# Kernel tuning notes

Measured on AMD Instinct MI355X. Metric: run time of the kernel, lower is better.

Reference implementation:

```python
import jax, jax.numpy as jnp
import numpy as np

NUM_COARSE = 1024

def sqdist(a, b):
    # a: [..., N, 3], b: [..., M, 3] -> [..., N, M] squared euclidean distances
    d = (jnp.sum(a * a, -1)[..., :, None] + jnp.sum(b * b, -1)[..., None, :]
         - 2.0 * jnp.einsum('...nd,...md->...nm', a, b))
    return jnp.maximum(d, 0.0)

def fps_idx(pts, n_samples):
    # pts: [N, 3]; farthest point sampling starting from index 0 (pn2 convention)
    d0 = jnp.sum((pts - pts[0]) ** 2, -1)  # [N]
    def step(dists, _):
        idx = jnp.argmax(dists)
        d = jnp.sum((pts - pts[idx]) ** 2, -1)
        return jnp.minimum(dists, d), idx
    _, idxs = jax.lax.scan(step, d0, None, length=n_samples - 1)
    return jnp.concatenate([jnp.zeros((1,), jnp.int32), idxs.astype(jnp.int32)])

def emd_dist(x, y, eps, iters):
    # x, y: [n, 3] equal-cardinality clouds. Approximate optimal assignment via
    # log-domain entropic OT (eps = regularization, iters = iterations), then
    # per-point squared distance to the matched point (as in the auction EMD kernel).
    n = x.shape[0]
    C = sqdist(x, y)                       # [n, n]
    Cs = jax.lax.stop_gradient(C)          # assignment is a constant wrt grads
    loga = -jnp.log(jnp.float32(n))
    def step(f, _):
        g = -eps * jax.nn.logsumexp((f[:, None] - Cs) / eps + loga, axis=0)
        f = -eps * jax.nn.logsumexp((g[None, :] - Cs) / eps + loga, axis=1)
        return f, None
    f, _ = jax.lax.scan(step, jnp.zeros((n,), Cs.dtype), None, length=iters)
    g = -eps * jax.nn.logsumexp((f[:, None] - Cs) / eps + loga, axis=0)
    assign = jnp.argmax(f[:, None] + g[None, :] - Cs, axis=1)  # [n]
    return jnp.take_along_axis(C, assign[:, None], axis=1)[:, 0]

def chamfer(a, b):
    # a: [B, N, 3], b: [B, M, 3] -> per-point min squared dists ([B,N], [B,M])
    C = sqdist(a, b)
    return jnp.min(C, axis=2), jnp.min(C, axis=1)

def setup_inputs() -> dict:
    key = jax.random.key(0)
    k1, k2, k3 = jax.random.split(key, 3)
    return {
        'output1': jax.random.uniform(k1, (4, NUM_COARSE, 3), jnp.float32),
        'output2': jax.random.uniform(k2, (4, 4096, 3), jnp.float32),
        'gt': jax.random.uniform(k3, (4, 4096, 3), jnp.float32),
        'eps': jnp.float32(0.005),
        'iters': 10,
    }

def reference(output1, output2, gt, eps, iters):
    gt = gt[:, :, :3]
    # --- EMD branch ---
    idx = jax.vmap(lambda p: fps_idx(p, NUM_COARSE))(gt)            # [B, num_coarse]
    gt_fps = jnp.take_along_axis(gt, idx[:, :, None], axis=1)       # [B, num_coarse, 3]
    d1 = jax.vmap(lambda x, y: emd_dist(x, y, eps, iters))(output1, gt_fps)
    emd1 = jnp.sqrt(d1).mean(1)
    d2 = jax.vmap(lambda x, y: emd_dist(x, y, eps, iters))(output2, gt)
    emd2 = jnp.sqrt(d2).mean(1)
    # --- Chamfer branch ---
    d11, d12 = chamfer(gt, output1)
    cd_p1 = (jnp.sqrt(d11).mean(1) + jnp.sqrt(d12).mean(1)) / 2
    cd_t1 = d11.mean(1) + d12.mean(1)
    d21, d22 = chamfer(gt, output2)
    cd_p2 = (jnp.sqrt(d21).mean(1) + jnp.sqrt(d22).mean(1)) / 2
    cd_t2 = d21.mean(1) + d22.mean(1)
    return (output1, output2, emd1, emd2, cd_p1, cd_p2, cd_t1, cd_t2)
```

## Files before the change

kernel.cpp:

```cpp
#include <hip/hip_runtime.h>
#include <math.h>


#define LOG2E 1.4426950408889634f
#define LN2   0.6931471805599453f
#define NEGBIG -3.0e38f

#define SY2(b) ((b) * 512)

#if __has_builtin(__builtin_amdgcn_exp2f)
__device__ __forceinline__ float fexp2(float x) { return __builtin_amdgcn_exp2f(x); }
#else
__device__ __forceinline__ float fexp2(float x) { return exp2f(x); }
#endif

__device__ __forceinline__ float dist_rn(float x, float y, float z,
                                         float qx, float qy, float qz) {
  float dx = __fsub_rn(x, qx), dy = __fsub_rn(y, qy), dz = __fsub_rn(z, qz);
  return __fadd_rn(__fadd_rn(__fmul_rn(dx, dx), __fmul_rn(dy, dy)),
                   __fmul_rn(dz, dz));
}

struct FpsS {
  float4 sq[4096];
  unsigned sVB[2][4];
  int sII[2][4];
  float4 sQ[2][4];
  float4 sOut[64];
};
struct WorkS {
  float4 ldsRow[256];
  float4 ldsC[1024];
  float ldsG2[1024];
  float red[8];
};
union SmemAll {
  FpsS f;
  WorkS w;
  float pad_force_one_block_per_cu[21504];
};

struct UniArgs {
  const float* gt;
  const float* epsP;
  const float4 *o1P4, *o2P4, *gtP4;
  float4* gfP4;
  float2 *gpart2, *fpart2, *apart2;
  unsigned* sync;
  float* out;
  int NC2, BPB;
};

__device__ __forceinline__ void bar_signal(unsigned* slot, unsigned val) {
  __syncthreads();
  if (threadIdx.x == 0)
    __hip_atomic_store(slot, val, __ATOMIC_RELEASE, __HIP_MEMORY_SCOPE_AGENT);
}
template <int SLP>
__device__ __forceinline__ void bar_waitall(const unsigned* base, int n,
                                            unsigned target) {
  if (threadIdx.x < 64) {
    int l = threadIdx.x;
    for (;;) {
      unsigned v = (l < n)
                       ? __hip_atomic_load(base + l * 16, __ATOMIC_RELAXED,
                                           __HIP_MEMORY_SCOPE_AGENT)
                       : target;
      if (__all((int)(v >= target))) break;
      __builtin_amdgcn_s_sleep(SLP);
    }
    if (l == 0)
      (void)__hip_atomic_load(base, __ATOMIC_ACQUIRE, __HIP_MEMORY_SCOPE_AGENT);
  }
  __syncthreads();
}

__device__ __forceinline__ float blockRedSum(float v, float* red4) {
#pragma unroll
  for (int m = 32; m; m >>= 1) v += __shfl_xor(v, m, 64);
  int lane = threadIdx.x & 63, wid = threadIdx.x >> 6;
  __syncthreads();
  if (lane == 0) red4[wid] = v;
  __syncthreads();
  float s = 0.0f;
  if (threadIdx.x == 0) {
#pragma unroll
    for (int w = 0; w < 4; ++w) s += red4[w];
  }
  return s;
}

__global__ __launch_bounds__(256) void prep_kernel(
    const float* __restrict__ o1, const float* __restrict__ o2,
    const float* __restrict__ gt, const float* __restrict__ epsP,
    float4* __restrict__ o1P4, float4* __restrict__ o2P4,
    float4* __restrict__ gtP4) {
  int id = blockIdx.x * 256 + threadIdx.x;
  float eps = *epsP;
  float se = (1.0f / eps) * LOG2E;
  float kxy = sqrtf(se + se);
  const float* src;
  float4* dst;
  if (id < 4096) { src = o1 + 3 * id; dst = o1P4 + id; }
  else if (id < 20480) { int p = id - 4096; src = o2 + 3 * p; dst = o2P4 + p; }
  else { int p = id - 20480; src = gt + 3 * p; dst = gtP4 + p; }
  float x = src[0], y = src[1], z = src[2];
  float xx = x * x + y * y + z * z;
  *dst = make_float4(kxy * x, kxy * y, kxy * z, xx * se);
}

template <int NC>
__device__ __forceinline__ float finalize_w(const float2* __restrict__ part,
                                            int gi, int stride, float nloga2) {
  float2 pp[NC];
#pragma unroll
  for (int c = 0; c < NC; ++c) pp[c] = part[c * stride + gi];
  float m = pp[0].x;
#pragma unroll
  for (int c = 1; c < NC; ++c) m = fmaxf(m, pp[c].x);
  float s = 0.0f;
#pragma unroll
  for (int c = 0; c < NC; ++c) s += pp[c].y * fexp2(pp[c].x - m);
  return nloga2 - (m + __log2f(s));
}

template <int NC>
__device__ void pass2_job(int b, int cb, int ch, const float4* __restrict__ rowP,
                          const float4* __restrict__ colP,
                          const float2* __restrict__ vpart,
                          float2* __restrict__ dst, float4* ldsRow) {
  const int CH = 4096 / NC;
  int tid = threadIdx.x;
  int gj = b * 4096 + cb * 2048 + tid;
  float cx[8], cy[8], cz[8];
#pragma unroll
  for (int c = 0; c < 8; ++c) {
    float4 cp = colP[gj + (c << 8)];
    cx[c] = cp.x; cy[c] = cp.y; cz[c] = cp.z;
  }
  float M[8], S[8];
#pragma unroll
  for (int c = 0; c < 8; ++c) { M[c] = NEGBIG; S[c] = 0.0f; }
  int r0 = ch * CH;
  for (int t0 = 0; t0 < CH; t0 += 256) {
    __syncthreads();
    {
      int gi = b * 4096 + r0 + t0 + tid;
      float4 rp = rowP[gi];
      float w = vpart ? finalize_w<NC>(vpart, gi, 16384, 12.0f) : -rp.w;
      ldsRow[tid] = make_float4(rp.x, rp.y, rp.z, w);
    }
    __syncthreads();
#pragma unroll 1
    for (int r = 0; r < 256; r += 8) {
      float4 q[8];
#pragma unroll
      for (int u = 0; u < 8; ++u) q[u] = ldsRow[r + u];
#pragma unroll
      for (int c = 0; c < 8; ++c) {
        float t[8];
#pragma unroll
        for (int u = 0; u < 8; ++u)
          t[u] = fmaf(cx[c], q[u].x, fmaf(cy[c], q[u].y, fmaf(cz[c], q[u].z, q[u].w)));
        float cm = fmaxf(fmaxf(fmaxf(t[0], t[1]), fmaxf(t[2], t[3])),
                         fmaxf(fmaxf(t[4], t[5]), fmaxf(t[6], t[7])));
        float nM = fmaxf(M[c], cm);
        float s8 = ((fexp2(t[0] - nM) + fexp2(t[1] - nM)) +
                    (fexp2(t[2] - nM) + fexp2(t[3] - nM))) +
                   ((fexp2(t[4] - nM) + fexp2(t[5] - nM)) +
                    (fexp2(t[6] - nM) + fexp2(t[7] - nM)));
        S[c] = fmaf(S[c], fexp2(M[c] - nM), s8);
        M[c] = nM;
      }
    }
  }
#pragma unroll
  for (int c = 0; c < 8; ++c)
    dst[ch * 16384 + gj + (c << 8)] = make_float2(M[c], S[c]);
}

__device__ void cham_job(const float4* __restrict__ aP, const float4* __restrict__ bP,
                         int Na, int Nb, float* outP, float* outT,
                         float scaleP, float scaleT, int b, int rb,
                         WorkS& w, const float* epsP) {
  int tid = threadIdx.x;
  int i0 = rb * 512 + tid, i1 = i0 + 256;
  float4 a0 = aP[b * Na + i0], a1 = aP[b * Na + i1];
  float m0 = 3.0e38f, m1 = 3.0e38f;
  for (int t0 = 0; t0 < Nb; t0 += 1024) {
    __syncthreads();
    for (int t = tid; t < 1024; t += 256) w.ldsC[t] = bP[b * Nb + t0 + t];
    __syncthreads();
#pragma unroll 4
    for (int t = 0; t < 1024; ++t) {
      float4 q = w.ldsC[t];
      float c0 = fmaf(-a0.z, q.z, fmaf(-a0.y, q.y, fmaf(-a0.x, q.x, q.w + a0.w)));
      float c1 = fmaf(-a1.z, q.z, fmaf(-a1.y, q.y, fmaf(-a1.x, q.x, q.w + a1.w)));
      m0 = fminf(m0, c0);
      m1 = fminf(m1, c1);
    }
  }
  float eps = *epsP;
  float inv_se = eps * LN2;
  float d0 = fmaxf(0.0f, m0 * inv_se), d1 = fmaxf(0.0f, m1 * inv_se);
  float s1 = blockRedSum(sqrtf(d0) + sqrtf(d1), w.red);
  float s2 = blockRedSum(d0 + d1, w.red);
  if (tid == 0) {
    atomicAdd(outP, s1 * scaleP);
    atomicAdd(outT, s2 * scaleT);
  }
}

__device__ void chamfer_worker(int g, const UniArgs& A, WorkS& w) {
  for (int cj = g; cj < 104; cj += 88) {
    if (cj < 32) {
      cham_job(A.gtP4, A.o2P4, 4096, 4096, A.out + 61452 + (cj >> 3),
               A.out + 61460 + (cj >> 3), 1.0f / 8192.0f, 1.0f / 4096.0f,
               cj >> 3, cj & 7, w, A.epsP);
    } else if (cj < 64) {
      int j = cj - 32;
      cham_job(A.o2P4, A.gtP4, 4096, 4096, A.out + 61452 + (j >> 3),
               A.out + 61460 + (j >> 3), 1.0f / 8192.0f, 1.0f / 4096.0f,
               j >> 3, j & 7, w, A.epsP);
    } else if (cj < 96) {
      int j = cj - 64;
      cham_job(A.gtP4, A.o1P4, 4096, 1024, A.out + 61448 + (j >> 3),
               A.out + 61456 + (j >> 3), 1.0f / 8192.0f, 1.0f / 4096.0f,
               j >> 3, j & 7, w, A.epsP);
    } else {
      int j = cj - 96;
      cham_job(A.o1P4, A.gtP4, 1024, 4096, A.out + 61448 + (j >> 1),
               A.out + 61456 + (j >> 1), 1.0f / 2048.0f, 1.0f / 1024.0f,
               j >> 1, j & 1, w, A.epsP);
    }
  }
}

template <int NC>
__device__ void assign2_job(int b, int cc, int rb, const UniArgs& A, WorkS& w) {
  int tid = threadIdx.x;
  __syncthreads();
  for (int t = tid; t < 1024; t += 256) {
    int gjc = b * 4096 + cc * 1024 + t;
    float wv = finalize_w<NC>(A.gpart2, gjc, 16384, 12.0f);
    float4 qp = A.gtP4[gjc];
    w.ldsC[t] = make_float4(qp.x, qp.y, qp.z, wv);
    w.ldsG2[t] = wv + qp.w;
  }
  __syncthreads();
#pragma unroll
  for (int rr = 0; rr < 2; ++rr) {
    int gi = b * 4096 + rb * 512 + (rr << 8) + tid;
    float4 rp = A.o2P4[gi];
    float rx = rp.x, ry = rp.y, rz = rp.z, xw = rp.w;
    float bW = NEGBIG;
    int bj = 0;
    for (int t = 0; t < 1024; ++t) {
      float4 q = w.ldsC[t];
      float W = fmaf(rz, q.z, fmaf(ry, q.y, fmaf(rx, q.x, q.w - xw)));
      W = fminf(W, w.ldsG2[t]);
      if (W > bW) { bW = W; bj = cc * 1024 + t; }
    }
    A.apart2[cc * 16384 + gi] = make_float2(bW, __int_as_float(bj));
  }
}

__device__ void combine2_job(int b, int rb, const UniArgs& A, WorkS& w) {
  int tid = threadIdx.x;
  int gi = b * 4096 + (rb << 8) + tid;
  float bW = NEGBIG;
  int bj = 0;
#pragma unroll
  for (int c = 0; c < 4; ++c) {
    float2 p = A.apart2[c * 16384 + gi];
    if (p.x > bW) { bW = p.x; bj = __float_as_int(p.y); }
  }
  float eps = *A.epsP;
  float inv_se = eps * LN2;
  float4 rp = A.o2P4[gi];
  float4 qp = A.gtP4[b * 4096 + bj];
  float dotp = rp.x * qp.x + rp.y * qp.y + rp.z * qp.z;
  float d = fmaxf(0.0f, (rp.w + qp.w - dotp) * inv_se);
  float s = blockRedSum(sqrtf(d), w.red);
  if (tid == 0) atomicAdd(A.out + 61444 + b, s * (1.0f / 4096.0f));
}

__device__ void fps_role(const UniArgs& A, int b, FpsS& f) {
  int tid = threadIdx.x;
  const float* base = A.gt + b * 12288;
  for (int t = tid; t < 4096; t += 256) {
    float x = base[3 * t], y = base[3 * t + 1], z = base[3 * t + 2];
    f.sq[t] = make_float4(x, y, z, x * x + y * y + z * z);
  }
  __syncthreads();
  float eps = *A.epsP;
  float se = (1.0f / eps) * LOG2E;
  float kxy = sqrtf(se + se);
  float4 p0 = f.sq[0];
  float px[16], py[16], pz[16], d[16];
#pragma unroll
  for (int k = 0; k < 16; ++k) {
    float4 p = f.sq[tid + (k << 8)];
    px[k] = p.x; py[k] = p.y; pz[k] = p.z;
    d[k] = dist_rn(p.x, p.y, p.z, p0.x, p0.y, p0.z);
  }
  if (tid == 0)
    f.sOut[0] = make_float4(kxy * p0.x, kxy * p0.y, kxy * p0.z, p0.w * se);
  int lane = tid & 63, wid = tid >> 6;
  float qx = p0.x, qy = p0.y, qz = p0.z;

#define DPPSTEP(C)                                                             \
  {                                                                            \
    unsigned ov = (unsigned)__builtin_amdgcn_update_dpp(0, (int)bvu, C, 0xf,  \
                                                        0xf, true);           \
    int oi = __builtin_amdgcn_update_dpp(0, bi, C, 0xf, 0xf, true);           \
    bool t = (ov > bvu) || ((ov == bvu) && ((unsigned)oi < (unsigned)bi));    \
    bvu = t ? ov : bvu;                                                        \
    bi = t ? oi : bi;                                                          \
  }
#define SCOMB(VV, II)                                                          \
  {                                                                            \
    unsigned _v = (unsigned)(VV);                                              \
    int _i = (II);                                                             \
    if (_v > wv || (_v == wv && _i < wi)) { wv = _v; wi = _i; }                \
  }
#define CCOMB(VV, II, QQ)                                                      \
  {                                                                            \
    unsigned _v = (VV);                                                        \
    int _i = (II);                                                             \
    bool t = (_v > v) || ((_v == v) && (_i < gsel));                           \
    v = t ? _v : v; gsel = t ? _i : gsel;                                      \
    nqx = t ? QQ.x : nqx; nqy = t ? QQ.y : nqy;                                \
    nqz = t ? QQ.z : nqz; nqw = t ? QQ.w : nqw;                                \
  }

  for (int s = 1; s < 1024; ++s) {
    float tv[8]; int ti[8];
#pragma unroll
    for (int i = 0; i < 8; ++i) {
      int k0 = 2 * i, k1 = 2 * i + 1;
      float n0 = fminf(d[k0], dist_rn(px[k0], py[k0], pz[k0], qx, qy, qz));
      float n1 = fminf(d[k1], dist_rn(px[k1], py[k1], pz[k1], qx, qy, qz));
      d[k0] = n0; d[k1] = n1;
      bool t = n1 > n0;
      tv[i] = t ? n1 : n0;
      ti[i] = tid + ((t ? k1 : k0) << 8);
    }
    float uv[4]; int ui[4];
#pragma unroll
    for (int i = 0; i < 4; ++i) {
      bool t = tv[2 * i + 1] > tv[2 * i];
      uv[i] = t ? tv[2 * i + 1] : tv[2 * i];
      ui[i] = t ? ti[2 * i + 1] : ti[2 * i];
    }
    bool tA = uv[1] > uv[0];
    float vA = tA ? uv[1] : uv[0]; int iA = tA ? ui[1] : ui[0];
    bool tB = uv[3] > uv[2];
    float vB = tB ? uv[3] : uv[2]; int iB = tB ? ui[3] : ui[2];
    bool tC = vB > vA;
    float bv = tC ? vB : vA; int bi = tC ? iB : iA;
    unsigned bvu = __float_as_uint(bv);
    DPPSTEP(0xB1)
    DPPSTEP(0x4E)
    DPPSTEP(0x141)
    DPPSTEP(0x140)
    unsigned wv = (unsigned)__builtin_amdgcn_readlane((int)bvu, 0);
    int wi = __builtin_amdgcn_readlane(bi, 0);
    SCOMB(__builtin_amdgcn_readlane((int)bvu, 16), __builtin_amdgcn_readlane(bi, 16))
    SCOMB(__builtin_amdgcn_readlane((int)bvu, 32), __builtin_amdgcn_readlane(bi, 32))
    SCOMB(__builtin_amdgcn_readlane((int)bvu, 48), __builtin_amdgcn_readlane(bi, 48))
    int par = s & 1;
    if (lane == 0) {
      f.sVB[par][wid] = wv;
      f.sII[par][wid] = wi;
      f.sQ[par][wid] = f.sq[wi];
    }
    __syncthreads();
    if ((s & 63) == 0 && tid < 64)
      A.gfP4[(b << 10) + (s - 64) + tid] = f.sOut[tid];
    unsigned v = f.sVB[par][0];
    int gsel = f.sII[par][0];
    float4 q0 = f.sQ[par][0], q1 = f.sQ[par][1];
    float4 q2 = f.sQ[par][2], q3 = f.sQ[par][3];
    float nqx = q0.x, nqy = q0.y, nqz = q0.z, nqw = q0.w;
    CCOMB(f.sVB[par][1], f.sII[par][1], q1)
    CCOMB(f.sVB[par][2], f.sII[par][2], q2)
    CCOMB(f.sVB[par][3], f.sII[par][3], q3)
    qx = nqx; qy = nqy; qz = nqz;
    if (tid == 0)
      f.sOut[s & 63] = make_float4(kxy * nqx, kxy * nqy, kxy * nqz, nqw * se);
  }
#undef DPPSTEP
#undef SCOMB
#undef CCOMB
  __syncthreads();
  if (tid < 64) A.gfP4[(b << 10) + 960 + tid] = f.sOut[tid];
}

__global__ __launch_bounds__(256, 1) void uni_kernel(UniArgs A) {
  __shared__ SmemAll sm;
  int bid = blockIdx.x;
  if (bid < 4) {
    fps_role(A, bid, sm.f);
    return;
  }
  int e = bid - 4;
  int W = 4 * A.BPB;
  if (e < W) {
    int b = e / A.BPB, rest = e % A.BPB;
    int cb = rest / A.NC2, ch = rest % A.NC2;
    unsigned* slots = A.sync + SY2(b);
    for (int s = 1; s <= 21; ++s) {
      const float4 *rowP, *colP;
      const float2* vp;
      float2* dst;
      if (s & 1) { rowP = A.o2P4; colP = A.gtP4; vp = (s == 1) ? nullptr : A.fpart2; dst = A.gpart2; }
      else       { rowP = A.gtP4; colP = A.o2P4; vp = A.gpart2; dst = A.fpart2; }
      if (A.NC2 == 16) pass2_job<16>(b, cb, ch, rowP, colP, vp, dst, sm.w.ldsRow);
      else             pass2_job<8>(b, cb, ch, rowP, colP, vp, dst, sm.w.ldsRow);
      bar_signal(slots + rest * 16, (unsigned)s);
      bar_waitall<16>(slots, A.BPB, (unsigned)s);
    }
    for (int j = rest; j < 32; j += A.BPB) {
      int cc = j >> 3, rb = j & 7;
      if (A.NC2 == 16) assign2_job<16>(b, cc, rb, A, sm.w);
      else             assign2_job<8>(b, cc, rb, A, sm.w);
    }
    bar_signal(slots + rest * 16, 22u);
    bar_waitall<4>(slots, A.BPB, 22u);
    if (rest < 16) combine2_job(b, rest, A, sm.w);
    return;
  }
  chamfer_worker(e - W, A, sm.w);
}

struct P1Args {
  const float4* rowP;
  const float4* colP;
  const float2* vpart;
  float2* dst;
};
__global__ __launch_bounds__(256) void pass1_kernel(P1Args J) {
  __shared__ float4 ldsRow[64];
  int b = blockIdx.x >> 4, ch = blockIdx.x & 15;
  int tid = threadIdx.x;
  int gj = b * 1024 + tid;
  float cx[4], cy[4], cz[4];
#pragma unroll
  for (int c = 0; c < 4; ++c) {
    float4 cp = J.colP[gj + (c << 8)];
    cx[c] = cp.x; cy[c] = cp.y; cz[c] = cp.z;
  }
  float M[4], S[4];
#pragma unroll
  for (int c = 0; c < 4; ++c) { M[c] = NEGBIG; S[c] = 0.0f; }
  int r0 = ch * 64;
  if (tid < 64) {
    int gi = b * 1024 + r0 + tid;
    float4 rp = J.rowP[gi];
    float w = J.vpart ? finalize_w<16>(J.vpart, gi, 4096, 10.0f) : -rp.w;
    ldsRow[tid] = make_float4(rp.x, rp.y, rp.z, w);
  }
  __syncthreads();
#pragma unroll 1
  for (int r = 0; r < 64; r += 8) {
    float4 q[8];
#pragma unroll
    for (int u = 0; u < 8; ++u) q[u] = ldsRow[r + u];
#pragma unroll
    for (int c = 0; c < 4; ++c) {
      float t[8];
#pragma unroll
      for (int u = 0; u < 8; ++u)
        t[u] = fmaf(cx[c], q[u].x, fmaf(cy[c], q[u].y, fmaf(cz[c], q[u].z, q[u].w)));
      float cm = fmaxf(fmaxf(fmaxf(t[0], t[1]), fmaxf(t[2], t[3])),
                       fmaxf(fmaxf(t[4], t[5]), fmaxf(t[6], t[7])));
      float nM = fmaxf(M[c], cm);
      float s8 = ((fexp2(t[0] - nM) + fexp2(t[1] - nM)) +
                  (fexp2(t[2] - nM) + fexp2(t[3] - nM))) +
                 ((fexp2(t[4] - nM) + fexp2(t[5] - nM)) +
                  (fexp2(t[6] - nM) + fexp2(t[7] - nM)));
      S[c] = fmaf(S[c], fexp2(M[c] - nM), s8);
      M[c] = nM;
    }
  }
#pragma unroll
  for (int c = 0; c < 4; ++c)
    J.dst[ch * 4096 + gj + (c << 8)] = make_float2(M[c], S[c]);
}

__global__ __launch_bounds__(256) void asg1_kernel(
    const float4* __restrict__ o1P4, const float4* __restrict__ gfP4,
    const float2* __restrict__ gpart1, const float* __restrict__ epsP,
    float* __restrict__ out) {
  __shared__ float4 ldsC[1024];
  __shared__ float ldsG2[1024];
  __shared__ float red[4];
  int b = blockIdx.x;
  int tid = threadIdx.x;
  for (int t = tid; t < 1024; t += 256) {
    int gjc = b * 1024 + t;
    float wv = finalize_w<16>(gpart1, gjc, 4096, 10.0f);
    float4 qp = gfP4[gjc];
    ldsC[t] = make_float4(qp.x, qp.y, qp.z, wv);
    ldsG2[t] = wv + qp.w;
  }
  __syncthreads();
  float eps = *epsP;
  float inv_se = eps * LN2;
  float vsum = 0.0f;
#pragma unroll
  for (int rr = 0; rr < 4; ++rr) {
    int gi = b * 1024 + (rr << 8) + tid;
    float4 rp = o1P4[gi];
    float rx = rp.x, ry = rp.y, rz = rp.z, xw = rp.w;
    float bW = NEGBIG;
    int bj = 0;
    for (int t = 0; t < 1024; ++t) {
      float4 q = ldsC[t];
      float W = fmaf(rz, q.z, fmaf(ry, q.y, fmaf(rx, q.x, q.w - xw)));
      W = fminf(W, ldsG2[t]);
      if (W > bW) { bW = W; bj = t; }
    }
    float4 qp = gfP4[b * 1024 + bj];
    float dotp = rp.x * qp.x + rp.y * qp.y + rp.z * qp.z;
    float d = fmaxf(0.0f, (rp.w + qp.w - dotp) * inv_se);
    vsum += sqrtf(d);
  }
  float s = blockRedSum(vsum, red);
  if (tid == 0) atomicAdd(out + 61440 + b, s * (1.0f / 1024.0f));
}

extern "C" void kernel_launch(void* const* d_in, const int* in_sizes, int n_in,
                              void* d_out, int out_size, void* d_ws, size_t ws_size,
                              hipStream_t stream) {
  (void)in_sizes; (void)n_in; (void)out_size;
  const float* o1 = (const float*)d_in[0];
  const float* o2 = (const float*)d_in[1];
  const float* gt = (const float*)d_in[2];
  const float* epsP = (const float*)d_in[3];
  float* out = (float*)d_out;
  float* ws = (float*)d_ws;

  int NC2 = 16;
  {
    size_t need16 = (size_t)(4096 + 16384 + 65536 + 65536 + 16384 +
                             2 * (16 * 32768) + 2 * 131072) * 4;
    if (ws_size < need16) NC2 = 8;
  }
  size_t off = 0;
  unsigned* syncp = (unsigned*)(ws + off); off += 4096;
  float4* o1P4 = (float4*)(ws + off); off += 16384;
  float4* o2P4 = (float4*)(ws + off); off += 65536;
  float4* gtP4 = (float4*)(ws + off); off += 65536;
  float4* gfP4 = (float4*)(ws + off); off += 16384;
  float2* gpart2 = (float2*)(ws + off); off += (size_t)NC2 * 32768;
  float2* fpart2 = (float2*)(ws + off); off += (size_t)NC2 * 32768;
  float2* apart2 = fpart2;
  float2* gpart1 = (float2*)(ws + off); off += 131072;
  float2* fpart1 = (float2*)(ws + off); off += 131072;

  (void)hipMemcpyAsync(out, o1, 12288 * sizeof(float), hipMemcpyDeviceToDevice, stream);
  (void)hipMemcpyAsync(out + 12288, o2, 49152 * sizeof(float), hipMemcpyDeviceToDevice, stream);
  (void)hipMemsetAsync(out + 61440, 0, 24 * sizeof(float), stream);
  (void)hipMemsetAsync(syncp, 0, 4096 * sizeof(unsigned), stream);

  prep_kernel<<<144, 256, 0, stream>>>(o1, o2, gt, epsP, o1P4, o2P4, gtP4);

  UniArgs A;
  A.gt = gt; A.epsP = epsP;
  A.o1P4 = o1P4; A.o2P4 = o2P4; A.gtP4 = gtP4; A.gfP4 = gfP4;
  A.gpart2 = gpart2; A.fpart2 = fpart2; A.apart2 = apart2;
  A.sync = syncp; A.out = out;
  A.NC2 = NC2; A.BPB = 2 * NC2;
  int grid = 4 + 4 * A.BPB + 88;
  uni_kernel<<<grid, 256, 0, stream>>>(A);

  for (int s = 1; s <= 21; ++s) {
    P1Args J;
    if (s & 1) { J.rowP = o1P4; J.colP = gfP4; J.vpart = (s == 1) ? nullptr : fpart1; J.dst = gpart1; }
    else       { J.rowP = gfP4; J.colP = o1P4; J.vpart = gpart1; J.dst = fpart1; }
    pass1_kernel<<<64, 256, 0, stream>>>(J);
  }
  asg1_kernel<<<4, 256, 0, stream>>>(o1P4, gfP4, gpart1, epsP, out);
}
```

Baseline: 1.339 ms.

## Fold coarse EMD Sinkhorn passes into persistent kernel with grid barriers

Removes the 21 separate pass1_kernel launches for the coarse EMD branch and runs those Sinkhorn iterations inside the persistent uni_kernel. The first 64 EMD2 worker blocks take this on after they finish their own work, waiting on a per-batch flag set by the FPS blocks. Each block keeps the row points in LDS and reduces its 16 partial log-sum-exp chunks locally into a finalized potential vector, so asg1 now reads one value per point. This trades launch overhead and partial-buffer traffic for running the coarse iterations serially after the EMD2 work, with 16-block spin barriers, which could lengthen the critical path.

```diff
diff --git a/kernel.cpp b/kernel.cpp
--- a/kernel.cpp
+++ b/kernel.cpp
@@ -7,6 +7,8 @@
 #define NEGBIG -3.0e38f
 
 #define SY2(b) ((b) * 512)
+#define SYF(b) (2048 + (b) * 16)
+#define SYE(b) (2176 + (b) * 256)
 
 #if __has_builtin(__builtin_amdgcn_exp2f)
 __device__ __forceinline__ float fexp2(float x) { return __builtin_amdgcn_exp2f(x); }
@@ -34,9 +36,15 @@
   float ldsG2[1024];
   float red[8];
 };
+struct Emd1S {
+  float4 rowsO[1024];
+  float4 rowsG[1024];
+  float2 part[64][17];
+};
 union SmemAll {
   FpsS f;
   WorkS w;
+  Emd1S e;
   float pad_force_one_block_per_cu[21504];
 };
 
@@ -46,6 +54,7 @@
   const float4 *o1P4, *o2P4, *gtP4;
   float4* gfP4;
   float2 *gpart2, *fpart2, *apart2;
+  float* vec1;
   unsigned* sync;
   float* out;
   int NC2, BPB;
@@ -395,6 +404,80 @@
 #undef CCOMB
   __syncthreads();
   if (tid < 64) A.gfP4[(b << 10) + 960 + tid] = f.sOut[tid];
+  bar_signal(A.sync + SYF(b), 1u);
+}
+
+__device__ void emd1_role(int eb, int chunk, const UniArgs& A, Emd1S& m) {
+  int tid = threadIdx.x;
+  bar_waitall<16>(A.sync + SYF(eb), 1, 1u);
+  for (int t = tid; t < 1024; t += 256) {
+    float4 p = A.o1P4[eb * 1024 + t];
+    m.rowsO[t] = make_float4(p.x, p.y, p.z, -p.w);
+    m.rowsG[t] = A.gfP4[eb * 1024 + t];
+  }
+  int col = chunk * 64 + (tid & 63);
+  int rl = tid >> 6;
+  float4 cG = A.gfP4[eb * 1024 + col];
+  float4 cO = A.o1P4[eb * 1024 + col];
+  float* gv = A.vec1 + (eb << 10);
+  float* fv = A.vec1 + 4096 + (eb << 10);
+  unsigned* slots = A.sync + SYE(eb);
+
+  for (int s = 1; s <= 21; ++s) {
+    int odd = s & 1;
+    if (s >= 2) {
+      const float* v = odd ? fv : gv;
+      float4* rows = odd ? m.rowsO : m.rowsG;
+      for (int t = tid; t < 1024; t += 256) rows[t].w = v[t];
+    }
+    __syncthreads();
+    const float4* rows = odd ? m.rowsO : m.rowsG;
+    float cx = odd ? cG.x : cO.x;
+    float cy = odd ? cG.y : cO.y;
+    float cz = odd ? cG.z : cO.z;
+#pragma unroll 1
+    for (int k = 0; k < 4; ++k) {
+      int ch = rl * 4 + k;
+      float M = NEGBIG, S = 0.0f;
+      int r0 = ch * 64;
+#pragma unroll 1
+      for (int r = 0; r < 64; r += 8) {
+        float4 q[8];
+#pragma unroll
+        for (int u = 0; u < 8; ++u) q[u] = rows[r0 + r + u];
+        float t8[8];
+#pragma unroll
+        for (int u = 0; u < 8; ++u)
+          t8[u] = fmaf(cx, q[u].x, fmaf(cy, q[u].y, fmaf(cz, q[u].z, q[u].w)));
+        float cm = fmaxf(fmaxf(fmaxf(t8[0], t8[1]), fmaxf(t8[2], t8[3])),
+                         fmaxf(fmaxf(t8[4], t8[5]), fmaxf(t8[6], t8[7])));
+        float nM = fmaxf(M, cm);
+        float s8 = ((fexp2(t8[0] - nM) + fexp2(t8[1] - nM)) +
+                    (fexp2(t8[2] - nM) + fexp2(t8[3] - nM))) +
+                   ((fexp2(t8[4] - nM) + fexp2(t8[5] - nM)) +
+                    (fexp2(t8[6] - nM) + fexp2(t8[7] - nM)));
+        S = fmaf(S, fexp2(M - nM), s8);
+        M = nM;
+      }
+      m.part[tid & 63][ch] = make_float2(M, S);
+    }
+    __syncthreads();
+    if (tid < 64) {
+      float2 pp[16];
+#pragma unroll
+      for (int c = 0; c < 16; ++c) pp[c] = m.part[tid][c];
+      float mm = pp[0].x;
+#pragma unroll
+      for (int c = 1; c < 16; ++c) mm = fmaxf(mm, pp[c].x);
+      float ss = 0.0f;
+#pragma unroll
+      for (int c = 0; c < 16; ++c) ss += pp[c].y * fexp2(pp[c].x - mm);
+      float w = 10.0f - (mm + __log2f(ss));
+      (odd ? gv : fv)[col] = w;
+    }
+    bar_signal(slots + chunk * 16, (unsigned)s);
+    bar_waitall<16>(slots, 16, (unsigned)s);
+  }
 }
 
 __global__ __launch_bounds__(256, 1) void uni_kernel(UniArgs A) {
@@ -429,69 +512,15 @@
     bar_signal(slots + rest * 16, 22u);
     bar_waitall<4>(slots, A.BPB, 22u);
     if (rest < 16) combine2_job(b, rest, A, sm.w);
+    if (e < 64) emd1_role(e >> 4, e & 15, A, sm.e);
     return;
   }
   chamfer_worker(e - W, A, sm.w);
-}
-
-struct P1Args {
-  const float4* rowP;
-  const float4* colP;
-  const float2* vpart;
-  float2* dst;
-};
-__global__ __launch_bounds__(256) void pass1_kernel(P1Args J) {
-  __shared__ float4 ldsRow[64];
-  int b = blockIdx.x >> 4, ch = blockIdx.x & 15;
-  int tid = threadIdx.x;
-  int gj = b * 1024 + tid;
-  float cx[4], cy[4], cz[4];
-#pragma unroll
-  for (int c = 0; c < 4; ++c) {
-    float4 cp = J.colP[gj + (c << 8)];
-    cx[c] = cp.x; cy[c] = cp.y; cz[c] = cp.z;
-  }
-  float M[4], S[4];
-#pragma unroll
-  for (int c = 0; c < 4; ++c) { M[c] = NEGBIG; S[c] = 0.0f; }
-  int r0 = ch * 64;
-  if (tid < 64) {
-    int gi = b * 1024 + r0 + tid;
-    float4 rp = J.rowP[gi];
-    float w = J.vpart ? finalize_w<16>(J.vpart, gi, 4096, 10.0f) : -rp.w;
-    ldsRow[tid] = make_float4(rp.x, rp.y, rp.z, w);
-  }
-  __syncthreads();
-#pragma unroll 1
-  for (int r = 0; r < 64; r += 8) {
-    float4 q[8];
-#pragma unroll
-    for (int u = 0; u < 8; ++u) q[u] = ldsRow[r + u];
-#pragma unroll
-    for (int c = 0; c < 4; ++c) {
-      float t[8];
-#pragma unroll
-      for (int u = 0; u < 8; ++u)
-        t[u] = fmaf(cx[c], q[u].x, fmaf(cy[c], q[u].y, fmaf(cz[c], q[u].z, q[u].w)));
-      float cm = fmaxf(fmaxf(fmaxf(t[0], t[1]), fmaxf(t[2], t[3])),
-                       fmaxf(fmaxf(t[4], t[5]), fmaxf(t[6], t[7])));
-      float nM = fmaxf(M[c], cm);
-      float s8 = ((fexp2(t[0] - nM) + fexp2(t[1] - nM)) +
-                  (fexp2(t[2] - nM) + fexp2(t[3] - nM))) +
-                 ((fexp2(t[4] - nM) + fexp2(t[5] - nM)) +
-                  (fexp2(t[6] - nM) + fexp2(t[7] - nM)));
-      S[c] = fmaf(S[c], fexp2(M[c] - nM), s8);
-      M[c] = nM;
-    }
-  }
-#pragma unroll
-  for (int c = 0; c < 4; ++c)
-    J.dst[ch * 4096 + gj + (c << 8)] = make_float2(M[c], S[c]);
 }
 
 __global__ __launch_bounds__(256) void asg1_kernel(
     const float4* __restrict__ o1P4, const float4* __restrict__ gfP4,
-    const float2* __restrict__ gpart1, const float* __restrict__ epsP,
+    const float* __restrict__ gvec, const float* __restrict__ epsP,
     float* __restrict__ out) {
   __shared__ float4 ldsC[1024];
   __shared__ float ldsG2[1024];
@@ -500,7 +529,7 @@
   int tid = threadIdx.x;
   for (int t = tid; t < 1024; t += 256) {
     int gjc = b * 1024 + t;
-    float wv = finalize_w<16>(gpart1, gjc, 4096, 10.0f);
+    float wv = gvec[gjc];
     float4 qp = gfP4[gjc];
     ldsC[t] = make_float4(qp.x, qp.y, qp.z, wv);
     ldsG2[t] = wv + qp.w;
@@ -557,8 +586,7 @@
   float2* gpart2 = (float2*)(ws + off); off += (size_t)NC2 * 32768;
   float2* fpart2 = (float2*)(ws + off); off += (size_t)NC2 * 32768;
   float2* apart2 = fpart2;
-  float2* gpart1 = (float2*)(ws + off); off += 131072;
-  float2* fpart1 = (float2*)(ws + off); off += 131072;
+  float* vec1 = (float*)(ws + off); off += 8192;
 
   (void)hipMemcpyAsync(out, o1, 12288 * sizeof(float), hipMemcpyDeviceToDevice, stream);
   (void)hipMemcpyAsync(out + 12288, o2, 49152 * sizeof(float), hipMemcpyDeviceToDevice, stream);
@@ -571,16 +599,11 @@
   A.gt = gt; A.epsP = epsP;
   A.o1P4 = o1P4; A.o2P4 = o2P4; A.gtP4 = gtP4; A.gfP4 = gfP4;
   A.gpart2 = gpart2; A.fpart2 = fpart2; A.apart2 = apart2;
+  A.vec1 = vec1;
   A.sync = syncp; A.out = out;
   A.NC2 = NC2; A.BPB = 2 * NC2;
   int grid = 4 + 4 * A.BPB + 88;
   uni_kernel<<<grid, 256, 0, stream>>>(A);
 
-  for (int s = 1; s <= 21; ++s) {
-    P1Args J;
-    if (s & 1) { J.rowP = o1P4; J.colP = gfP4; J.vpart = (s == 1) ? nullptr : fpart1; J.dst = gpart1; }
-    else       { J.rowP = gfP4; J.colP = o1P4; J.vpart = gpart1; J.dst = fpart1; }
-    pass1_kernel<<<64, 256, 0, stream>>>(J);
-  }
-  asg1_kernel<<<4, 256, 0, stream>>>(o1P4, gfP4, gpart1, epsP, out);
-}
+  asg1_kernel<<<4, 256, 0, stream>>>(o1P4, gfP4, vec1, epsP, out);
+}
```

After: 1.420 ms. +6.0%, slower.
